# Kernel tuning notes

Hardware: AMD Instinct MI355X
Metric: run time of the kernel (lower is better)

Reference implementation:

```python
import jax, jax.numpy as jnp
import numpy as np

EMBED_DIM = 768
NUM_HEADS = 12
HEAD_DIM = EMBED_DIM // NUM_HEADS
MAX_WAVELENGTH = 10000.0
ROPE_PERCENT = 0.5


def p_rope(x, positions):
    """Partial RoPE (Gemma-style half-split layout) on x: [BH, S, D]."""
    rope_angles = int(ROPE_PERCENT * HEAD_DIM) // 2
    nope_angles = HEAD_DIM // 2 - rope_angles
    fraction = 2.0 * jnp.arange(rope_angles, dtype=x.dtype) / HEAD_DIM
    timescale = MAX_WAVELENGTH ** fraction
    # infinite timescale => angle 0 => identity rotation for the non-roped dims
    timescale = jnp.concatenate([timescale, jnp.full((nope_angles,), jnp.inf, dtype=x.dtype)])
    sinusoid = positions[:, None] / timescale[None, :]  # [S, D/2]
    sin, cos = jnp.sin(sinusoid), jnp.cos(sinusoid)
    x1, x2 = jnp.split(x, 2, axis=-1)  # each [BH, S, D/2]
    return jnp.concatenate([x1 * cos - x2 * sin, x2 * cos + x1 * sin], axis=-1)


def setup_inputs() -> dict:
    key = jax.random.key(0)
    ks = jax.random.split(key, 9)
    B, T, E = 16, 1024, EMBED_DIM
    s = 0.02
    return {
        "hidden_states": jax.random.normal(ks[0], (B, T, E), jnp.float32),
        "wq": jax.random.normal(ks[1], (E, E), jnp.float32) * s,
        "bq": jax.random.normal(ks[2], (E,), jnp.float32) * s,
        "wk": jax.random.normal(ks[3], (E, E), jnp.float32) * s,
        "bk": jax.random.normal(ks[4], (E,), jnp.float32) * s,
        "wv": jax.random.normal(ks[5], (E, E), jnp.float32) * s,
        "bv": jax.random.normal(ks[6], (E,), jnp.float32) * s,
        "wo": jax.random.normal(ks[7], (E, E), jnp.float32) * s,
        "bo": jax.random.normal(ks[8], (E,), jnp.float32) * s,
    }


def _shape(x, B, S):
    # [B, S, E] -> [B*H, S, head_dim]
    return x.reshape(B, S, NUM_HEADS, HEAD_DIM).transpose(0, 2, 1, 3).reshape(B * NUM_HEADS, S, HEAD_DIM)


def reference(hidden_states, wq, bq, wk, bk, wv, bv, wo, bo):
    B, T, E = hidden_states.shape
    scaling = HEAD_DIM ** -0.5
    # torch nn.Linear: y = x @ W.T + b
    q = (hidden_states @ wq.T + bq) * scaling
    k = hidden_states @ wk.T + bk
    v = hidden_states @ wv.T + bv
    q = _shape(q, B, T)  # [BH, T, D]
    k = _shape(k, B, T)
    v = _shape(v, B, T)
    positions = jnp.arange(T, dtype=hidden_states.dtype)
    k = p_rope(k, positions)
    q = p_rope(q, positions)
    attn = jnp.einsum('bqd,bkd->bqk', q, k)  # [BH, T, T]
    attn = jax.nn.softmax(attn, axis=-1)
    out = jnp.einsum('bqk,bkd->bqd', attn, v)  # [BH, T, D]
    out = out.reshape(B, NUM_HEADS, T, HEAD_DIM).transpose(0, 2, 1, 3).reshape(B, T, E)
    return out @ wo.T + bo
```

## Files before the change

kernel.cpp:

```cpp
#include <hip/hip_runtime.h>
#include <hip/hip_bf16.h>
#include <math.h>

typedef __hip_bfloat16 bf16;
typedef __attribute__((ext_vector_type(8))) __bf16 bf16x8;
typedef __attribute__((ext_vector_type(8))) unsigned short u16x8;
typedef __attribute__((ext_vector_type(4))) float f32x4;
typedef __attribute__((ext_vector_type(16))) float f32x16;
typedef unsigned int u32;
typedef __attribute__((ext_vector_type(4))) unsigned int u32x4;

#define DEVI static __device__ __forceinline__

#define BATCH 16
#define SEQ 1024
#define EMB 768
#define NHEAD 12
#define HDIM 64
#define BHEADS (BATCH * NHEAD)
#define MROWS (BATCH * SEQ)

DEVI f32x4 mfma16x16(bf16x8 a, bf16x8 b, f32x4 c) {
  return __builtin_amdgcn_mfma_f32_16x16x32_bf16(a, b, c, 0, 0, 0);
}
DEVI f32x16 mfma32x32(bf16x8 a, bf16x8 b, f32x16 c) {
  return __builtin_amdgcn_mfma_f32_32x32x16_bf16(a, b, c, 0, 0, 0);
}

DEVI void gload_lds16(const bf16* g, void* lds) {
  __builtin_amdgcn_global_load_lds(
      (const __attribute__((address_space(1))) void*)g,
      (__attribute__((address_space(3))) void*)lds, 16, 0, 0);
}

#if __has_builtin(__builtin_amdgcn_exp2f)
DEVI float fexp2(float x) { return __builtin_amdgcn_exp2f(x); }
#else
DEVI float fexp2(float x) { return exp2f(x); }
#endif

DEVI unsigned short f2bf_bits(float f) {
  bf16 h = __float2bfloat16(f);
  return *reinterpret_cast<unsigned short*>(&h);
}
DEVI u32 pack2(float lo, float hi) {
  return (u32)f2bf_bits(lo) | ((u32)f2bf_bits(hi) << 16);
}

__global__ __launch_bounds__(256) void convert_bf16_kernel(
    const float* __restrict__ src, bf16* __restrict__ dst, int n8) {
  int i = blockIdx.x * 256 + threadIdx.x;
  if (i >= n8) return;
  const float4* s = (const float4*)src + (long)i * 2;
  float4 a = s[0], b = s[1];
  u16x8 r;
  r[0] = f2bf_bits(a.x); r[1] = f2bf_bits(a.y);
  r[2] = f2bf_bits(a.z); r[3] = f2bf_bits(a.w);
  r[4] = f2bf_bits(b.x); r[5] = f2bf_bits(b.y);
  r[6] = f2bf_bits(b.z); r[7] = f2bf_bits(b.w);
  *(u16x8*)(dst + (long)i * 8) = r;
}

__global__ void rope_table_kernel(float2* __restrict__ tbl) {
  int i = blockIdx.x * 256 + threadIdx.x;
  if (i >= SEQ * 16) return;
  int t = i >> 4;
  int d = i & 15;
  double inv_ts = pow(10000.0, -(double)d / 32.0);
  double ang = (double)t * inv_ts;
  tbl[i] = make_float2((float)cos(ang), (float)sin(ang));
}

DEVI void gemm_core_768(const bf16* __restrict__ A, const bf16* __restrict__ Bt,
                        int rowBase, int colBase, bf16* Asm, bf16* Bsm,
                        f32x4 (&acc)[4][4]) {
  const int K = 768;
  const int tid = threadIdx.x;
  const int wave = tid >> 6;
  const int lane = tid & 63;
  const int c0 = lane & 15;
  const int khi = lane >> 4;
  const int wm = wave >> 1, wn = wave & 1;
  const int srow = tid >> 2;
  const int scol = (tid & 3) * 8;
  const bf16* aG = A + (long)(rowBase + srow) * K + scol;
  const bf16* bG = Bt + (long)(colBase + srow) * K + scol;
  char* aL0 = (char*)Asm + wave * 1024;
  char* aL1 = (char*)Asm + 4096 + wave * 1024;
  char* bL0 = (char*)Bsm + wave * 1024;
  char* bL1 = (char*)Bsm + 4096 + wave * 1024;
  const int stride64 = 64 * K;

#define G_STAGE(boff, kk)                                                    \
  gload_lds16(aG + (kk), aL0 + (boff));                                      \
  gload_lds16(aG + stride64 + (kk), aL1 + (boff));                           \
  gload_lds16(bG + (kk), bL0 + (boff));                                      \
  gload_lds16(bG + stride64 + (kk), bL1 + (boff));

#define G_COMPUTE(be)                                                        \
  {                                                                          \
    bf16x8 af[4], bfr[4];                                                    \
    _Pragma("unroll") for (int m = 0; m < 4; ++m) af[m] =                    \
        *(const bf16x8*)(Asm + (be) + (wm * 64 + m * 16 + c0) * 32 + khi * 8); \
    _Pragma("unroll") for (int n = 0; n < 4; ++n) bfr[n] =                   \
        *(const bf16x8*)(Bsm + (be) + (wn * 64 + n * 16 + c0) * 32 + khi * 8); \
    _Pragma("unroll") for (int m = 0; m < 4; ++m)                            \
      _Pragma("unroll") for (int n = 0; n < 4; ++n)                          \
        acc[m][n] = mfma16x16(af[m], bfr[n], acc[m][n]);                     \
  }

  G_STAGE(0, 0);
  asm volatile("s_waitcnt vmcnt(0)" ::: "memory");
  __syncthreads();

  for (int kk = 0; kk < K; kk += 64) {
    G_STAGE(8192, kk + 32);
    G_COMPUTE(0);
    asm volatile("s_waitcnt vmcnt(0)" ::: "memory");
    __syncthreads();
    if (kk + 64 < K) { G_STAGE(0, kk + 64); }
    G_COMPUTE(4096);
    asm volatile("s_waitcnt vmcnt(0)" ::: "memory");
    __syncthreads();
  }
#undef G_STAGE
#undef G_COMPUTE
}

__global__ __launch_bounds__(256) void qkv_kernel(
    const bf16* __restrict__ hs,
    const bf16* __restrict__ wq, const float* __restrict__ bq,
    const bf16* __restrict__ wk, const float* __restrict__ bk,
    const bf16* __restrict__ wv, const float* __restrict__ bv,
    const float2* __restrict__ tbl,
    bf16* __restrict__ Qb, bf16* __restrict__ Kb, bf16* __restrict__ Vtb) {
  __shared__ __align__(16) bf16 Asm[2 * 128 * 32];
  __shared__ __align__(16) bf16 Bsm[2 * 128 * 32];
  const int type = blockIdx.z;
  const bf16* W = (type == 0) ? wq : (type == 1) ? wk : wv;
  const float* bias = (type == 0) ? bq : (type == 1) ? bk : bv;
  const int rowBase = blockIdx.x * 128;
  const int colBase = blockIdx.y * 128;
  f32x4 acc[4][4] = {};
  gemm_core_768(hs, W, rowBase, colBase, Asm, Bsm, acc);

  const int tid = threadIdx.x;
  const int wave = tid >> 6, lane = tid & 63;
  const int c0 = lane & 15, khi = lane >> 4;
  const int wm = wave >> 1, wn = wave & 1;
  const int colW = colBase + wn * 64;
  const int head = colW >> 6;
  float bb[4];
#pragma unroll
  for (int n = 0; n < 4; ++n) bb[n] = bias[colW + n * 16 + c0];

  const int rW = rowBase + wm * 64;
  const int bIdx = rW >> 10;
  const int bh = bIdx * NHEAD + head;

  if (type == 2) {
#pragma unroll
    for (int m = 0; m < 4; ++m) {
      const int t0 = (rW & 1023) + m * 16 + khi * 4;
#pragma unroll
      for (int n = 0; n < 4; ++n) {
        const int d = n * 16 + c0;
        bf16* vp = Vtb + ((long)bh * HDIM + d) * SEQ + t0;
        ushort4 pk;
        pk.x = f2bf_bits(acc[m][n][0] + bb[n]);
        pk.y = f2bf_bits(acc[m][n][1] + bb[n]);
        pk.z = f2bf_bits(acc[m][n][2] + bb[n]);
        pk.w = f2bf_bits(acc[m][n][3] + bb[n]);
        *(ushort4*)vp = pk;
      }
    }
  } else {
    const float scl = (type == 0) ? 0.125f * 1.44269504f : 1.0f;
    bf16* base = ((type == 0) ? Qb : Kb) + (long)bh * SEQ * HDIM;
#pragma unroll
    for (int m = 0; m < 4; ++m) {
#pragma unroll
      for (int ri = 0; ri < 4; ++ri) {
        const int t = (rW & 1023) + m * 16 + khi * 4 + ri;
        float v0 = (acc[m][0][ri] + bb[0]) * scl;
        float v1 = (acc[m][1][ri] + bb[1]) * scl;
        float v2 = (acc[m][2][ri] + bb[2]) * scl;
        float v3 = (acc[m][3][ri] + bb[3]) * scl;
        const float2 cs = tbl[t * 16 + c0];
        const float r0 = v0 * cs.x - v2 * cs.y;
        const float r2 = v2 * cs.x + v0 * cs.y;
        bf16* qp = base + (long)t * HDIM;
        qp[c0] = __float2bfloat16(r0);
        qp[16 + c0] = __float2bfloat16(v1);
        qp[32 + c0] = __float2bfloat16(r2);
        qp[48 + c0] = __float2bfloat16(v3);
      }
    }
  }
}


DEVI int swoff(int row, int s) {
  return row * 128 + (((s ^ (row & 7)) & 7) << 4);
}

__global__ __launch_bounds__(256, 2) void attn_kernel(
    const bf16* __restrict__ Q, const bf16* __restrict__ K,
    const bf16* __restrict__ Vt, bf16* __restrict__ Ao) {
  __shared__ __align__(16) char smem[4 * 8192];
  const int bid = blockIdx.x;
  const int xcd = bid & 7, idx = bid >> 3;
  const int bh = xcd + ((idx >> 2) << 3);
  const int qt = idx & 3;

  const int tid = threadIdx.x;
  const int lane = tid & 63;
  const int w = tid >> 6;
  const int l31 = lane & 31;
  const int hi = lane >> 5;

  const bf16* Qh = Q + (long)bh * SEQ * HDIM;
  const bf16* Kh = K + (long)bh * SEQ * HDIM;
  const bf16* Vh = Vt + (long)bh * HDIM * SEQ;

  const int qbase = qt * 256 + w * 64;
  bf16x8 qf[2][4];
#pragma unroll
  for (int qn = 0; qn < 2; ++qn)
#pragma unroll
    for (int ks = 0; ks < 4; ++ks)
      qf[qn][ks] = *(const bf16x8*)(Qh + (qbase + qn * 32 + l31) * HDIM +
                                    ks * 16 + hi * 8);

  f32x16 o[2][2] = {};
  float lacc[2] = {0.f, 0.f};

  const int sr = tid >> 3;
  const int sc = tid & 7;

  bf16x8 kr0 = *(const bf16x8*)(Kh + sr * HDIM + sc * 8);
  bf16x8 kr1 = *(const bf16x8*)(Kh + (sr + 32) * HDIM + sc * 8);
  bf16x8 vr0 = *(const bf16x8*)(Vh + sr * SEQ + sc * 8);
  bf16x8 vr1 = *(const bf16x8*)(Vh + (sr + 32) * SEQ + sc * 8);
  *(bf16x8*)(smem + swoff(sr, sc)) = kr0;
  *(bf16x8*)(smem + swoff(sr + 32, sc)) = kr1;
  *(bf16x8*)(smem + 16384 + swoff(sr, sc)) = vr0;
  *(bf16x8*)(smem + 16384 + swoff(sr + 32, sc)) = vr1;
  __syncthreads();

  for (int ct = 0; ct < SEQ / 64; ++ct) {
    const int co = (ct & 1) * 8192;
    const char* Kc = smem + co;
    const char* Vc = smem + 16384 + co;

    if (ct != 15) {
      const int nt = (ct + 1) * 64;
      kr0 = *(const bf16x8*)(Kh + (nt + sr) * HDIM + sc * 8);
      kr1 = *(const bf16x8*)(Kh + (nt + sr + 32) * HDIM + sc * 8);
      vr0 = *(const bf16x8*)(Vh + sr * SEQ + nt + sc * 8);
      vr1 = *(const bf16x8*)(Vh + (sr + 32) * SEQ + nt + sc * 8);
    }

    f32x16 s[2][2] = {};
#pragma unroll
    for (int m = 0; m < 2; ++m)
#pragma unroll
      for (int ks = 0; ks < 4; ++ks) {
        bf16x8 ka = *(const bf16x8*)(Kc + swoff(m * 32 + l31, ks * 2 + hi));
        s[m][0] = mfma32x32(ka, qf[0][ks], s[m][0]);
        s[m][1] = mfma32x32(ka, qf[1][ks], s[m][1]);
      }

    bf16x8 pf[2][4];
#pragma unroll
    for (int qn = 0; qn < 2; ++qn) {
      u32 wds[2][4][2];
#pragma unroll
      for (int m = 0; m < 2; ++m)
#pragma unroll
        for (int b = 0; b < 4; ++b)
#pragma unroll
          for (int pp = 0; pp < 2; ++pp) {
            const float p0 = fexp2(s[m][qn][4 * b + 2 * pp]);
            const float p1 = fexp2(s[m][qn][4 * b + 2 * pp + 1]);
            lacc[qn] += p0 + p1;
            wds[m][b][pp] = pack2(p0, p1);
          }
#pragma unroll
      for (int m = 0; m < 2; ++m)
#pragma unroll
        for (int ts = 0; ts < 2; ++ts) {
          u32 x0 = wds[m][2 * ts][0], y0 = wds[m][2 * ts + 1][0];
          u32 x1 = wds[m][2 * ts][1], y1 = wds[m][2 * ts + 1][1];
          asm("v_permlane32_swap_b32 %0, %1" : "+v"(x0), "+v"(y0));
          asm("v_permlane32_swap_b32 %0, %1" : "+v"(x1), "+v"(y1));
          u32x4 t = {x0, x1, y0, y1};
          pf[qn][2 * m + ts] = *(bf16x8*)&t;
        }
    }

#pragma unroll
    for (int dm = 0; dm < 2; ++dm)
#pragma unroll
      for (int tk = 0; tk < 4; ++tk) {
        bf16x8 va = *(const bf16x8*)(Vc + swoff(dm * 32 + l31, tk * 2 + hi));
        o[dm][0] = mfma32x32(va, pf[0][tk], o[dm][0]);
        o[dm][1] = mfma32x32(va, pf[1][tk], o[dm][1]);
      }

    if (ct != 15) {
      const int no = 8192 - co;
      *(bf16x8*)(smem + no + swoff(sr, sc)) = kr0;
      *(bf16x8*)(smem + no + swoff(sr + 32, sc)) = kr1;
      *(bf16x8*)(smem + 16384 + no + swoff(sr, sc)) = vr0;
      *(bf16x8*)(smem + 16384 + no + swoff(sr + 32, sc)) = vr1;
      __syncthreads();
    }
  }

#pragma unroll
  for (int qn = 0; qn < 2; ++qn) lacc[qn] += __shfl_xor(lacc[qn], 32);
  const float inv0 = 1.0f / lacc[0];
  const float inv1 = 1.0f / lacc[1];

  const int bb = bh / NHEAD;
  const int hh = bh % NHEAD;
#pragma unroll
  for (int qn = 0; qn < 2; ++qn) {
    const float inv = qn ? inv1 : inv0;
    const int t = qbase + qn * 32 + l31;
    bf16* orow = Ao + (long)(bb * SEQ + t) * EMB + hh * HDIM;
#pragma unroll
    for (int dm = 0; dm < 2; ++dm)
#pragma unroll
      for (int b = 0; b < 4; ++b)
#pragma unroll
        for (int pp = 0; pp < 2; ++pp) {
          const int r = 4 * b + 2 * pp;
          const int d = dm * 32 + 2 * pp + 8 * b + 4 * hi;
          *(u32*)(orow + d) = pack2(o[dm][qn][r] * inv, o[dm][qn][r + 1] * inv);
        }
  }
}

__global__ __launch_bounds__(256) void oproj_kernel(
    const bf16* __restrict__ X, const bf16* __restrict__ wo,
    const float* __restrict__ bo, float* __restrict__ out) {
  __shared__ __align__(16) bf16 Asm[2 * 128 * 32];
  __shared__ __align__(16) bf16 Bsm[2 * 128 * 32];
  const int rowBase = blockIdx.x * 128;
  const int colBase = blockIdx.y * 128;
  f32x4 acc[4][4] = {};
  gemm_core_768(X, wo, rowBase, colBase, Asm, Bsm, acc);
  const int tid = threadIdx.x;
  const int wave = tid >> 6, lane = tid & 63;
  const int c0 = lane & 15, khi = lane >> 4;
  const int wm = wave >> 1, wn = wave & 1;
  const int colW = colBase + wn * 64;
  float bb[4];
#pragma unroll
  for (int n = 0; n < 4; ++n) bb[n] = bo[colW + n * 16 + c0];
#pragma unroll
  for (int m = 0; m < 4; ++m)
#pragma unroll
    for (int ri = 0; ri < 4; ++ri) {
      const int row = rowBase + wm * 64 + m * 16 + khi * 4 + ri;
      float* op = out + (long)row * EMB + colW;
#pragma unroll
      for (int n = 0; n < 4; ++n)
        op[n * 16 + c0] = acc[m][n][ri] + bb[n];
    }
}

extern "C" void kernel_launch(void* const* d_in, const int* in_sizes, int n_in,
                              void* d_out, int out_size, void* d_ws, size_t ws_size,
                              hipStream_t stream) {
  const float* hs_f = (const float*)d_in[0];
  const float* wq_f = (const float*)d_in[1];
  const float* bq = (const float*)d_in[2];
  const float* wk_f = (const float*)d_in[3];
  const float* bk = (const float*)d_in[4];
  const float* wv_f = (const float*)d_in[5];
  const float* bv = (const float*)d_in[6];
  const float* wo_f = (const float*)d_in[7];
  const float* bo = (const float*)d_in[8];
  float* out = (float*)d_out;

  char* ws = (char*)d_ws;
  size_t off = 0;
  float2* tbl = (float2*)ws; off += 131072;
  const size_t hsBytes = (size_t)MROWS * EMB * 2;
  const size_t wBytes = (size_t)EMB * EMB * 2;
  const size_t bufBytes = (size_t)BHEADS * SEQ * HDIM * 2;
  bf16* hsb = (bf16*)(ws + off); off += hsBytes;
  bf16* wqb = (bf16*)(ws + off); off += wBytes;
  bf16* wkb = (bf16*)(ws + off); off += wBytes;
  bf16* wvb = (bf16*)(ws + off); off += wBytes;
  bf16* wob = (bf16*)(ws + off); off += wBytes;
  bf16* Qb = (bf16*)(ws + off); off += bufBytes;
  bf16* Kb = (bf16*)(ws + off); off += bufBytes;
  bf16* Vtb = (bf16*)(ws + off); off += bufBytes;
  bf16* Ao = (bf16*)(ws + off);

  const int nHs8 = MROWS * EMB / 8;
  const int nW8 = EMB * EMB / 8;
  convert_bf16_kernel<<<dim3(nHs8 / 256), dim3(256), 0, stream>>>(hs_f, hsb, nHs8);
  convert_bf16_kernel<<<dim3(nW8 / 256), dim3(256), 0, stream>>>(wq_f, wqb, nW8);
  convert_bf16_kernel<<<dim3(nW8 / 256), dim3(256), 0, stream>>>(wk_f, wkb, nW8);
  convert_bf16_kernel<<<dim3(nW8 / 256), dim3(256), 0, stream>>>(wv_f, wvb, nW8);
  convert_bf16_kernel<<<dim3(nW8 / 256), dim3(256), 0, stream>>>(wo_f, wob, nW8);
  rope_table_kernel<<<dim3(64), dim3(256), 0, stream>>>(tbl);
  qkv_kernel<<<dim3(MROWS / 128, EMB / 128, 3), dim3(256), 0, stream>>>(
      hsb, wqb, bq, wkb, bk, wvb, bv, tbl, Qb, Kb, Vtb);
  attn_kernel<<<dim3(768), dim3(256), 0, stream>>>(Qb, Kb, Vtb, Ao);
  oproj_kernel<<<dim3(MROWS / 128, EMB / 128), dim3(256), 0, stream>>>(Ao, wob, bo, out);
}
```

Baseline: 212.8 us.

## Triple-buffer GEMM K-loop with partial vmcnt waits and single barrier per tile

Replaces the double-buffered K loop of the shared 768-K GEMM core with a three-stage LDS ring. Loads are issued two tiles ahead, and each phase waits only for the older tile (vmcnt(4)) before a single barrier, instead of draining all loads and syncing twice per step. LDS per block grows by half, and launch bounds request three blocks per SM to limit register use. It relies on the hand-tuned waitcnt count matching the four loads per stage, and the occupancy hint may cause register spills.

```diff
diff --git a/kernel.cpp b/kernel.cpp
--- a/kernel.cpp
+++ b/kernel.cpp
@@ -75,6 +75,7 @@
                         int rowBase, int colBase, bf16* Asm, bf16* Bsm,
                         f32x4 (&acc)[4][4]) {
   const int K = 768;
+  const int NT = 24;
   const int tid = threadIdx.x;
   const int wave = tid >> 6;
   const int lane = tid & 63;
@@ -109,33 +110,41 @@
         acc[m][n] = mfma16x16(af[m], bfr[n], acc[m][n]);                     \
   }
 
+#define G_PHASE(beElem, sByte, tc)                                           \
+  {                                                                          \
+    if ((tc) + 1 < NT) {                                                     \
+      asm volatile("s_waitcnt vmcnt(4)" ::: "memory");                       \
+    } else {                                                                 \
+      asm volatile("s_waitcnt vmcnt(0)" ::: "memory");                       \
+    }                                                                        \
+    __builtin_amdgcn_s_barrier();                                            \
+    __builtin_amdgcn_sched_barrier(0);                                       \
+    if ((tc) + 2 < NT) { G_STAGE(sByte, ((tc) + 2) * 32); }                  \
+    G_COMPUTE(beElem);                                                       \
+  }
+
   G_STAGE(0, 0);
-  asm volatile("s_waitcnt vmcnt(0)" ::: "memory");
-  __syncthreads();
-
-  for (int kk = 0; kk < K; kk += 64) {
-    G_STAGE(8192, kk + 32);
-    G_COMPUTE(0);
-    asm volatile("s_waitcnt vmcnt(0)" ::: "memory");
-    __syncthreads();
-    if (kk + 64 < K) { G_STAGE(0, kk + 64); }
-    G_COMPUTE(4096);
-    asm volatile("s_waitcnt vmcnt(0)" ::: "memory");
-    __syncthreads();
-  }
+  G_STAGE(8192, 32);
+
+  for (int tt = 0; tt < NT; tt += 3) {
+    G_PHASE(0, 16384, tt);
+    G_PHASE(4096, 0, tt + 1);
+    G_PHASE(8192, 8192, tt + 2);
+  }
+#undef G_PHASE
 #undef G_STAGE
 #undef G_COMPUTE
 }
 
-__global__ __launch_bounds__(256) void qkv_kernel(
+__global__ __launch_bounds__(256, 3) void qkv_kernel(
     const bf16* __restrict__ hs,
     const bf16* __restrict__ wq, const float* __restrict__ bq,
     const bf16* __restrict__ wk, const float* __restrict__ bk,
     const bf16* __restrict__ wv, const float* __restrict__ bv,
     const float2* __restrict__ tbl,
     bf16* __restrict__ Qb, bf16* __restrict__ Kb, bf16* __restrict__ Vtb) {
-  __shared__ __align__(16) bf16 Asm[2 * 128 * 32];
-  __shared__ __align__(16) bf16 Bsm[2 * 128 * 32];
+  __shared__ __align__(16) bf16 Asm[3 * 128 * 32];
+  __shared__ __align__(16) bf16 Bsm[3 * 128 * 32];
   const int type = blockIdx.z;
   const bf16* W = (type == 0) ? wq : (type == 1) ? wk : wv;
   const float* bias = (type == 0) ? bq : (type == 1) ? bk : bv;
@@ -343,11 +352,11 @@
   }
 }
 
-__global__ __launch_bounds__(256) void oproj_kernel(
+__global__ __launch_bounds__(256, 3) void oproj_kernel(
     const bf16* __restrict__ X, const bf16* __restrict__ wo,
     const float* __restrict__ bo, float* __restrict__ out) {
-  __shared__ __align__(16) bf16 Asm[2 * 128 * 32];
-  __shared__ __align__(16) bf16 Bsm[2 * 128 * 32];
+  __shared__ __align__(16) bf16 Asm[3 * 128 * 32];
+  __shared__ __align__(16) bf16 Bsm[3 * 128 * 32];
   const int rowBase = blockIdx.x * 128;
   const int colBase = blockIdx.y * 128;
   f32x4 acc[4][4] = {};
```

Measured after the change: 191.6 us. 1.11x faster.
